# Kernel optimization log

Measured on AMD Instinct MI355X. Metric: run time of the kernel, lower is better.

## Reference

```python
import jax, jax.numpy as jnp
import numpy as np

B, N, D, E = 256, 192, 512, 1024
H = E // 2          # MLP hidden = 512
K = 58              # round(0.3 * 192), hardcoded in the torch forward
EPS_L2 = 1e-8
EPS_BN = 1e-5


def setup_inputs() -> dict:
    key = jax.random.key(0)
    ks = jax.random.split(key, 8)
    s = 0.02
    return {
        "all_patch_embeddings": jax.random.normal(ks[0], (B, N, D), dtype=jnp.float32),
        "attention_map": jax.random.uniform(ks[1], (B, N + 1, N + 1), dtype=jnp.float32),
        # fc: Linear(D, E)
        "W_fc": jax.random.normal(ks[2], (E, D), dtype=jnp.float32) * s,
        "b_fc": jnp.zeros((E,), dtype=jnp.float32),
        # mlp layer 0: Linear(D, H) + BatchNorm1d(H) + ReLU
        "W1": jax.random.normal(ks[3], (H, D), dtype=jnp.float32) * s,
        "b1": jnp.zeros((H,), dtype=jnp.float32),
        "gamma1": jnp.ones((H,), dtype=jnp.float32),
        "beta1": jnp.zeros((H,), dtype=jnp.float32),
        # mlp layer 1: Linear(H, E) (no BN/ReLU applied on last layer)
        "W2": jax.random.normal(ks[4], (E, H), dtype=jnp.float32) * s,
        "b2": jnp.zeros((E,), dtype=jnp.float32),
    }


def reference(all_patch_embeddings, attention_map, W_fc, b_fc, W1, b1, gamma1, beta1, W2, b2):
    # CLS-row attention over the 192 patch tokens: [B, N]
    cls_attn = attention_map[:, 0, 1:]
    # torch.sort(descending)[...,:K] == top-k indices (batched, replaces python loop)
    _, idx = jax.lax.top_k(cls_attn, K)                      # [B, K] int32
    # batched gather replacing the per-sample index_select loop
    sel = jnp.take_along_axis(all_patch_embeddings, idx[:, :, None], axis=1)  # [B, K, D]
    # l2norm over last dim
    norm = jnp.sqrt(jnp.sum(sel * sel, axis=-1, keepdims=True)) + EPS_L2
    base = sel / norm
    # .half() cast in the original (round-trip to fp16 precision)
    base = base.astype(jnp.float16).astype(jnp.float32)
    # fc branch
    feat_fc = jnp.einsum('bkd,ed->bke', base, W_fc) + b_fc    # [B, K, E]
    # mlp branch (num_layers=2): Linear -> BN(train-mode batch stats) -> ReLU -> Linear
    h = jnp.einsum('bkd,hd->bkh', base, W1) + b1              # [B, K, H]
    hf = h.reshape(B * K, H)
    mu = jnp.mean(hf, axis=0)
    var = jnp.var(hf, axis=0)
    hf = (hf - mu) * jax.lax.rsqrt(var + EPS_BN) * gamma1 + beta1
    h = jax.nn.relu(hf).reshape(B, K, H)
    feat_mlp = jnp.einsum('bkh,eh->bke', h, W2) + b2          # [B, K, E]
    feats = feat_mlp + feat_fc
    # maxk_pool1d_var with k=1 and lengths == K reduces to max over token dim
    return jnp.max(feats, axis=1).astype(jnp.float32)         # [B, E]
```

## Files before the change

kernel.cpp:

```cpp
#include <hip/hip_runtime.h>
#include <hip/hip_fp16.h>

#define B_ 256
#define N_ 192
#define D_ 512
#define E_ 1024
#define H_ 512
#define K_ 58
#define M_ (B_*K_)
#define M2_ (B_*64)

typedef _Float16 f16;
typedef unsigned int u32;
typedef _Float16 half8 __attribute__((ext_vector_type(8)));
typedef float floatx4 __attribute__((ext_vector_type(4)));

__device__ inline half8 cvt8(float4 f0, float4 f1) {
  half8 r;
  r[0]=(f16)f0.x; r[1]=(f16)f0.y; r[2]=(f16)f0.z; r[3]=(f16)f0.w;
  r[4]=(f16)f1.x; r[5]=(f16)f1.y; r[6]=(f16)f1.z; r[7]=(f16)f1.w;
  return r;
}

__device__ inline void gl_lds16(const f16* g, f16* l) {
  __builtin_amdgcn_global_load_lds((const __attribute__((address_space(1))) u32*)g,
                                   (__attribute__((address_space(3))) u32*)l, 16, 0, 0);
}

__device__ inline void stage128(const f16* gbase, int gstride, f16* sT, int w, int lane) {
  int lrow  = lane >> 2;
  int chunk = (lane & 3) ^ ((lane >> 3) & 3);
  gl_lds16(gbase + (size_t)(w*16      + lrow)*gstride + chunk*8, &sT[(w*16)*32]);
  gl_lds16(gbase + (size_t)(64 + w*16 + lrow)*gstride + chunk*8, &sT[(64 + w*16)*32]);
}

__global__ void setup_kernel(const float* __restrict__ Wfc, const float* __restrict__ W2,
                             const float* __restrict__ W1, const float* __restrict__ attn,
                             const float* __restrict__ emb,
                             f16* __restrict__ Wcat, f16* __restrict__ W1_16,
                             f16* __restrict__ A16, float* __restrict__ csum) {
  __shared__ float sv[N_];
  __shared__ int sidx[K_];
  __shared__ int cnt;
  int blk = blockIdx.x, t = threadIdx.x;
  if (blk < 512) {
    int idx = (blk*256 + t)*8;
    int e = idx >> 10, c = idx & 1023;
    const float* src = (c < 512) ? (Wfc + (size_t)e*512 + c)
                                 : (W2  + (size_t)e*512 + (c-512));
    half8 o = cvt8(((const float4*)src)[0], ((const float4*)src)[1]);
    *(uint4*)(Wcat + idx) = *(uint4*)&o;
  } else if (blk < 640) {
    int idx = ((blk-512)*256 + t)*8;
    const float* src = W1 + idx;
    half8 o = cvt8(((const float4*)src)[0], ((const float4*)src)[1]);
    *(uint4*)(W1_16 + idx) = *(uint4*)&o;
  } else if (blk < 896) {
    int b = blk - 640;
    if (t == 0) cnt = 0;
    if (t < N_) sv[t] = attn[(size_t)b*193*193 + 1 + t];
    __syncthreads();
    if (t < N_) {
      float v = sv[t]; int rank = 0;
      for (int j = 0; j < N_; ++j) {
        float vj = sv[j];
        rank += (vj > v) || (vj == v && j < t);
      }
      if (rank < K_) sidx[atomicAdd(&cnt, 1)] = t;
    }
    __syncthreads();
    int w = t >> 6, lane = t & 63;
    for (int slot = w; slot < 64; slot += 4) {
      f16* dst = A16 + ((size_t)b*64 + slot)*1024 + lane*8;
      if (slot < K_) {
        const float* src = emb + ((size_t)b*N_ + sidx[slot])*D_ + lane*8;
        float4 v0 = ((const float4*)src)[0];
        float4 v1 = ((const float4*)src)[1];
        float s = v0.x*v0.x + v0.y*v0.y + v0.z*v0.z + v0.w*v0.w
                + v1.x*v1.x + v1.y*v1.y + v1.z*v1.z + v1.w*v1.w;
        #pragma unroll
        for (int off = 32; off > 0; off >>= 1) s += __shfl_xor(s, off);
        float inv = 1.0f / (sqrtf(s) + 1e-8f);
        half8 o;
        o[0]=(f16)(v0.x*inv); o[1]=(f16)(v0.y*inv); o[2]=(f16)(v0.z*inv); o[3]=(f16)(v0.w*inv);
        o[4]=(f16)(v1.x*inv); o[5]=(f16)(v1.y*inv); o[6]=(f16)(v1.z*inv); o[7]=(f16)(v1.w*inv);
        *(uint4*)dst = *(uint4*)&o;
      } else {
        uint4 z; z.x=0u; z.y=0u; z.z=0u; z.w=0u;
        *(uint4*)dst = z;
      }
    }
  } else {
    float4 z; z.x=0.f; z.y=0.f; z.z=0.f; z.w=0.f;
    ((float4*)csum)[t] = z;
  }
}

__launch_bounds__(256)
__global__ void gemm1_kernel(const f16* __restrict__ A16, const f16* __restrict__ W1_16,
                             const float* __restrict__ b1, f16* __restrict__ Aout,
                             float* __restrict__ csum, float* __restrict__ css) {
  __shared__ f16 sA[2][128*32];
  __shared__ f16 sB[2][128*32];
  __shared__ float sSum[4][64], sSS[4][64];
  int t = threadIdx.x;
  int n0 = blockIdx.x * 128;
  int m0 = blockIdx.y * 128;
  int lane = t & 63, w = t >> 6, lm = lane & 15, quad = lane >> 4;
  int rh = w & 1, ch = w >> 1;
  floatx4 acc[4][4] = {};
  const f16* Ab = A16 + (size_t)m0*1024;
  const f16* Bb = W1_16 + (size_t)n0*512;
  int sw = (quad ^ ((lm >> 1) & 3)) * 8;
  stage128(Ab, 1024, sA[0], w, lane);
  stage128(Bb, 512,  sB[0], w, lane);
  __syncthreads();
  for (int it = 0; it < 16; ++it) {
    int cur = it & 1, nxt = cur ^ 1;
    if (it < 15) {
      stage128(Ab + (it+1)*32, 1024, sA[nxt], w, lane);
      stage128(Bb + (it+1)*32, 512,  sB[nxt], w, lane);
    }
    half8 a[4], bf[4];
    #pragma unroll
    for (int i = 0; i < 4; ++i) a[i]  = *(const half8*)&sA[cur][(rh*64 + i*16 + lm)*32 + sw];
    #pragma unroll
    for (int j = 0; j < 4; ++j) bf[j] = *(const half8*)&sB[cur][(ch*64 + j*16 + lm)*32 + sw];
    #pragma unroll
    for (int i = 0; i < 4; ++i)
      #pragma unroll
      for (int j = 0; j < 4; ++j)
        acc[i][j] = __builtin_amdgcn_mfma_f32_16x16x32_f16(a[i], bf[j], acc[i][j], 0, 0, 0);
    __syncthreads();
  }
  #pragma unroll
  for (int j = 0; j < 4; ++j) {
    int col = n0 + ch*64 + j*16 + lm;
    float bias = b1[col];
    float s = 0.f, ss = 0.f;
    #pragma unroll
    for (int i = 0; i < 4; ++i) {
      int rib = i*16 + quad*4;
      int row = m0 + rh*64 + rib;
      #pragma unroll
      for (int r = 0; r < 4; ++r) {
        float x = acc[i][j][r] + bias;
        Aout[(size_t)(row + r)*1024 + 512 + col] = (f16)x;
        if (rib + r < K_) { s += x; ss += x*x; }
      }
    }
    s  += __shfl_xor(s, 16);  s  += __shfl_xor(s, 32);
    ss += __shfl_xor(ss, 16); ss += __shfl_xor(ss, 32);
    if (lane < 16) { sSum[w][j*16 + lm] = s; sSS[w][j*16 + lm] = ss; }
  }
  __syncthreads();
  if (t < 128) {
    int wp = (t >> 6) * 2, ci = t & 63;
    atomicAdd(&csum[n0 + t], sSum[wp][ci] + sSum[wp+1][ci]);
    atomicAdd(&css[n0 + t],  sSS[wp][ci]  + sSS[wp+1][ci]);
  }
}

__global__ void bnrelu_kernel(f16* __restrict__ A16, const float* __restrict__ csum,
                              const float* __restrict__ css, const float* __restrict__ gamma,
                              const float* __restrict__ beta) {
  __shared__ float sSc[H_], sSh[H_];
  int t = threadIdx.x;
  for (int j = t; j < H_; j += 256) {
    float mu  = csum[j] * (1.0f/M_);
    float var = css[j] * (1.0f/M_) - mu*mu;
    float sc  = gamma[j] * rsqrtf(var + 1e-5f);
    sSc[j] = sc;
    sSh[j] = beta[j] - mu*sc;
  }
  __syncthreads();
  int r0 = blockIdx.x * 16;
  #pragma unroll
  for (int i = 0; i < 4; ++i) {
    int seg = t + 256*i;
    int row = r0 + (seg >> 6);
    int c0  = (seg & 63) * 8;
    f16* p = A16 + (size_t)row*1024 + 512 + c0;
    if ((row & 63) >= K_) {
      uint4 z; z.x=0u; z.y=0u; z.z=0u; z.w=0u;
      *(uint4*)p = z;
    } else {
      half8 hv = *(const half8*)p;
      half8 o;
      #pragma unroll
      for (int k = 0; k < 8; ++k)
        o[k] = (f16)fmaxf((float)hv[k]*sSc[c0+k] + sSh[c0+k], 0.0f);
      *(uint4*)p = *(uint4*)&o;
    }
  }
}

__launch_bounds__(256)
__global__ void fused_kernel(const f16* __restrict__ A16, const f16* __restrict__ Wcat,
                             const float* __restrict__ bfc, const float* __restrict__ b2,
                             float* __restrict__ out) {
  __shared__ f16 sA[2][128*32];
  __shared__ f16 sB[2][128*32];
  __shared__ float sMax[4][64];
  int t = threadIdx.x;
  int e0 = blockIdx.x * 128;
  int bm = blockIdx.y;
  int lane = t & 63, w = t >> 6, lm = lane & 15, quad = lane >> 4;
  int rh = w & 1, ch = w >> 1;
  floatx4 acc[4][4] = {};
  const f16* Ab = A16 + (size_t)bm*128*1024;
  const f16* Bb = Wcat + (size_t)e0*1024;
  int sw = (quad ^ ((lm >> 1) & 3)) * 8;
  stage128(Ab, 1024, sA[0], w, lane);
  stage128(Bb, 1024, sB[0], w, lane);
  __syncthreads();
  for (int it = 0; it < 32; ++it) {
    int cur = it & 1, nxt = cur ^ 1;
    if (it < 31) {
      stage128(Ab + (it+1)*32, 1024, sA[nxt], w, lane);
      stage128(Bb + (it+1)*32, 1024, sB[nxt], w, lane);
    }
    half8 a[4], bf[4];
    #pragma unroll
    for (int i = 0; i < 4; ++i) a[i]  = *(const half8*)&sA[cur][(rh*64 + i*16 + lm)*32 + sw];
    #pragma unroll
    for (int j = 0; j < 4; ++j) bf[j] = *(const half8*)&sB[cur][(ch*64 + j*16 + lm)*32 + sw];
    #pragma unroll
    for (int i = 0; i < 4; ++i)
      #pragma unroll
      for (int j = 0; j < 4; ++j)
        acc[i][j] = __builtin_amdgcn_mfma_f32_16x16x32_f16(a[i], bf[j], acc[i][j], 0, 0, 0);
    __syncthreads();
  }
  #pragma unroll
  for (int j = 0; j < 4; ++j) {
    float mx = -3.0e38f;
    #pragma unroll
    for (int i = 0; i < 4; ++i) {
      int rib = i*16 + quad*4;
      #pragma unroll
      for (int r = 0; r < 4; ++r)
        if (rib + r < K_) mx = fmaxf(mx, acc[i][j][r]);
    }
    mx = fmaxf(mx, __shfl_xor(mx, 16));
    mx = fmaxf(mx, __shfl_xor(mx, 32));
    if (lane < 16) sMax[w][j*16 + lm] = mx;
  }
  __syncthreads();
  {
    int bb = t >> 7, c = t & 127;
    float mx = sMax[(c >> 6)*2 + bb][c & 63];
    int e = e0 + c;
    out[((size_t)bm*2 + bb)*E_ + e] = mx + bfc[e] + b2[e];
  }
}

extern "C" void kernel_launch(void* const* d_in, const int* in_sizes, int n_in,
                              void* d_out, int out_size, void* d_ws, size_t ws_size,
                              hipStream_t stream) {
  const float* emb   = (const float*)d_in[0];
  const float* attn  = (const float*)d_in[1];
  const float* Wfc   = (const float*)d_in[2];
  const float* bfc   = (const float*)d_in[3];
  const float* W1    = (const float*)d_in[4];
  const float* b1    = (const float*)d_in[5];
  const float* gamma = (const float*)d_in[6];
  const float* beta  = (const float*)d_in[7];
  const float* W2    = (const float*)d_in[8];
  const float* b2    = (const float*)d_in[9];
  float* out = (float*)d_out;

  char* ws = (char*)d_ws;
  f16*   A16   = (f16*)(ws);
  f16*   Wcat  = (f16*)(ws + 33554432);
  f16*   W1_16 = (f16*)(ws + 35651584);
  float* csum  = (float*)(ws + 36175872);
  float* css   = (float*)(ws + 36177920);

  setup_kernel<<<897, 256, 0, stream>>>(Wfc, W2, W1, attn, emb, Wcat, W1_16, A16, csum);
  gemm1_kernel<<<dim3(H_/128, M2_/128), 256, 0, stream>>>(A16, W1_16, b1, A16, csum, css);
  bnrelu_kernel<<<M2_/16, 256, 0, stream>>>(A16, csum, css, gamma, beta);
  fused_kernel<<<dim3(E_/128, M2_/128), 256, 0, stream>>>(A16, Wcat, bfc, b2, out);
}
```

Measured before the change: 249.9 us.

## Widen GEMM tiles to 128x256 and remap blocks for XCD-aware locality

Both GEMM kernels now compute 128x256 output tiles per block, so each wave holds a 4x8 grid of MFMA accumulators. This halves A-tile reloads and raises the arithmetic intensity per LDS read. The launch switches to a 1D grid whose block-to-tile mapping places blocks sharing the same A rows on the same XCD (blockIdx & 7), aiming for better L2 reuse. In exchange, register pressure and LDS use go up, and block count halves (256 and 512 blocks), which may limit occupancy and wave-level parallelism.

New measurement: 248.6 us. No clear change (-0.5%).

```diff
diff --git a/kernel.cpp b/kernel.cpp
--- a/kernel.cpp
+++ b/kernel.cpp
@@ -32,6 +32,13 @@
   int chunk = (lane & 3) ^ ((lane >> 3) & 3);
   gl_lds16(gbase + (size_t)(w*16      + lrow)*gstride + chunk*8, &sT[(w*16)*32]);
   gl_lds16(gbase + (size_t)(64 + w*16 + lrow)*gstride + chunk*8, &sT[(64 + w*16)*32]);
+}
+__device__ inline void stage256(const f16* gbase, int gstride, f16* sT, int w, int lane) {
+  int lrow  = lane >> 2;
+  int chunk = (lane & 3) ^ ((lane >> 3) & 3);
+  #pragma unroll
+  for (int q = 0; q < 4; ++q)
+    gl_lds16(gbase + (size_t)(q*64 + w*16 + lrow)*gstride + chunk*8, &sT[(q*64 + w*16)*32]);
 }
 
 __global__ void setup_kernel(const float* __restrict__ Wfc, const float* __restrict__ W2,
@@ -96,52 +103,55 @@
   }
 }
 
-__launch_bounds__(256)
+__launch_bounds__(256, 2)
 __global__ void gemm1_kernel(const f16* __restrict__ A16, const f16* __restrict__ W1_16,
                              const float* __restrict__ b1, f16* __restrict__ Aout,
                              float* __restrict__ csum, float* __restrict__ css) {
   __shared__ f16 sA[2][128*32];
-  __shared__ f16 sB[2][128*32];
-  __shared__ float sSum[4][64], sSS[4][64];
+  __shared__ f16 sB[2][256*32];
+  __shared__ float sSum[4][128], sSS[4][128];
   int t = threadIdx.x;
-  int n0 = blockIdx.x * 128;
-  int m0 = blockIdx.y * 128;
+  int g = blockIdx.x;
+  int xcd = g & 7, rest = g >> 3;
+  int n0 = (rest & 1) * 256;
+  int m  = xcd + 8*(rest >> 1);
+  int m0 = m * 128;
   int lane = t & 63, w = t >> 6, lm = lane & 15, quad = lane >> 4;
-  int rh = w & 1, ch = w >> 1;
-  floatx4 acc[4][4] = {};
+  int rw = w & 1, cw = w >> 1;
+  floatx4 acc[4][8] = {};
   const f16* Ab = A16 + (size_t)m0*1024;
   const f16* Bb = W1_16 + (size_t)n0*512;
   int sw = (quad ^ ((lm >> 1) & 3)) * 8;
   stage128(Ab, 1024, sA[0], w, lane);
-  stage128(Bb, 512,  sB[0], w, lane);
+  stage256(Bb, 512,  sB[0], w, lane);
   __syncthreads();
   for (int it = 0; it < 16; ++it) {
     int cur = it & 1, nxt = cur ^ 1;
     if (it < 15) {
       stage128(Ab + (it+1)*32, 1024, sA[nxt], w, lane);
-      stage128(Bb + (it+1)*32, 512,  sB[nxt], w, lane);
-    }
-    half8 a[4], bf[4];
-    #pragma unroll
-    for (int i = 0; i < 4; ++i) a[i]  = *(const half8*)&sA[cur][(rh*64 + i*16 + lm)*32 + sw];
-    #pragma unroll
-    for (int j = 0; j < 4; ++j) bf[j] = *(const half8*)&sB[cur][(ch*64 + j*16 + lm)*32 + sw];
+      stage256(Bb + (it+1)*32, 512,  sB[nxt], w, lane);
+    }
+    half8 a[4], bf[8];
+    #pragma unroll
+    for (int i = 0; i < 4; ++i) a[i]  = *(const half8*)&sA[cur][(rw*64  + i*16 + lm)*32 + sw];
+    #pragma unroll
+    for (int j = 0; j < 8; ++j) bf[j] = *(const half8*)&sB[cur][(cw*128 + j*16 + lm)*32 + sw];
     #pragma unroll
     for (int i = 0; i < 4; ++i)
       #pragma unroll
-      for (int j = 0; j < 4; ++j)
+      for (int j = 0; j < 8; ++j)
         acc[i][j] = __builtin_amdgcn_mfma_f32_16x16x32_f16(a[i], bf[j], acc[i][j], 0, 0, 0);
     __syncthreads();
   }
   #pragma unroll
-  for (int j = 0; j < 4; ++j) {
-    int col = n0 + ch*64 + j*16 + lm;
+  for (int j = 0; j < 8; ++j) {
+    int col = n0 + cw*128 + j*16 + lm;
     float bias = b1[col];
     float s = 0.f, ss = 0.f;
     #pragma unroll
     for (int i = 0; i < 4; ++i) {
       int rib = i*16 + quad*4;
-      int row = m0 + rh*64 + rib;
+      int row = m0 + rw*64 + rib;
       #pragma unroll
       for (int r = 0; r < 4; ++r) {
         float x = acc[i][j][r] + bias;
@@ -154,10 +164,11 @@
     if (lane < 16) { sSum[w][j*16 + lm] = s; sSS[w][j*16 + lm] = ss; }
   }
   __syncthreads();
-  if (t < 128) {
-    int wp = (t >> 6) * 2, ci = t & 63;
-    atomicAdd(&csum[n0 + t], sSum[wp][ci] + sSum[wp+1][ci]);
-    atomicAdd(&css[n0 + t],  sSS[wp][ci]  + sSS[wp+1][ci]);
+  {
+    int c = t;
+    int w0 = 2*(c >> 7), ci = c & 127;
+    atomicAdd(&csum[n0 + c], sSum[w0][ci] + sSum[w0+1][ci]);
+    atomicAdd(&css[n0 + c],  sSS[w0][ci]  + sSS[w0+1][ci]);
   }
 }
 
@@ -195,45 +206,47 @@
   }
 }
 
-__launch_bounds__(256)
+__launch_bounds__(256, 2)
 __global__ void fused_kernel(const f16* __restrict__ A16, const f16* __restrict__ Wcat,
                              const float* __restrict__ bfc, const float* __restrict__ b2,
                              float* __restrict__ out) {
   __shared__ f16 sA[2][128*32];
-  __shared__ f16 sB[2][128*32];
-  __shared__ float sMax[4][64];
+  __shared__ f16 sB[2][256*32];
+  __shared__ float sMax[4][128];
   int t = threadIdx.x;
-  int e0 = blockIdx.x * 128;
-  int bm = blockIdx.y;
+  int g = blockIdx.x;
+  int xcd = g & 7, rest = g >> 3;
+  int e0 = (rest & 3) * 256;
+  int bm = xcd + 8*(rest >> 2);
   int lane = t & 63, w = t >> 6, lm = lane & 15, quad = lane >> 4;
-  int rh = w & 1, ch = w >> 1;
-  floatx4 acc[4][4] = {};
+  int rw = w & 1, cw = w >> 1;
+  floatx4 acc[4][8] = {};
   const f16* Ab = A16 + (size_t)bm*128*1024;
   const f16* Bb = Wcat + (size_t)e0*1024;
   int sw = (quad ^ ((lm >> 1) & 3)) * 8;
   stage128(Ab, 1024, sA[0], w, lane);
-  stage128(Bb, 1024, sB[0], w, lane);
+  stage256(Bb, 1024, sB[0], w, lane);
   __syncthreads();
   for (int it = 0; it < 32; ++it) {
     int cur = it & 1, nxt = cur ^ 1;
     if (it < 31) {
       stage128(Ab + (it+1)*32, 1024, sA[nxt], w, lane);
-      stage128(Bb + (it+1)*32, 1024, sB[nxt], w, lane);
-    }
-    half8 a[4], bf[4];
-    #pragma unroll
-    for (int i = 0; i < 4; ++i) a[i]  = *(const half8*)&sA[cur][(rh*64 + i*16 + lm)*32 + sw];
-    #pragma unroll
-    for (int j = 0; j < 4; ++j) bf[j] = *(const half8*)&sB[cur][(ch*64 + j*16 + lm)*32 + sw];
+      stage256(Bb + (it+1)*32, 1024, sB[nxt], w, lane);
+    }
+    half8 a[4], bf[8];
+    #pragma unroll
+    for (int i = 0; i < 4; ++i) a[i]  = *(const half8*)&sA[cur][(rw*64  + i*16 + lm)*32 + sw];
+    #pragma unroll
+    for (int j = 0; j < 8; ++j) bf[j] = *(const half8*)&sB[cur][(cw*128 + j*16 + lm)*32 + sw];
     #pragma unroll
     for (int i = 0; i < 4; ++i)
       #pragma unroll
-      for (int j = 0; j < 4; ++j)
+      for (int j = 0; j < 8; ++j)
         acc[i][j] = __builtin_amdgcn_mfma_f32_16x16x32_f16(a[i], bf[j], acc[i][j], 0, 0, 0);
     __syncthreads();
   }
   #pragma unroll
-  for (int j = 0; j < 4; ++j) {
+  for (int j = 0; j < 8; ++j) {
     float mx = -3.0e38f;
     #pragma unroll
     for (int i = 0; i < 4; ++i) {
@@ -247,9 +260,10 @@
     if (lane < 16) sMax[w][j*16 + lm] = mx;
   }
   __syncthreads();
-  {
-    int bb = t >> 7, c = t & 127;
-    float mx = sMax[(c >> 6)*2 + bb][c & 63];
+  #pragma unroll
+  for (int bb = 0; bb < 2; ++bb) {
+    int c = t;
+    float mx = sMax[bb + 2*(c >> 7)][c & 127];
     int e = e0 + c;
     out[((size_t)bm*2 + bb)*E_ + e] = mx + bfc[e] + b2[e];
   }
@@ -278,7 +292,7 @@
   float* css   = (float*)(ws + 36177920);
 
   setup_kernel<<<897, 256, 0, stream>>>(Wfc, W2, W1, attn, emb, Wcat, W1_16, A16, csum);
-  gemm1_kernel<<<dim3(H_/128, M2_/128), 256, 0, stream>>>(A16, W1_16, b1, A16, csum, css);
+  gemm1_kernel<<<256, 256, 0, stream>>>(A16, W1_16, b1, A16, csum, css);
   bnrelu_kernel<<<M2_/16, 256, 0, stream>>>(A16, csum, css, gamma, beta);
-  fused_kernel<<<dim3(E_/128, M2_/128), 256, 0, stream>>>(A16, Wcat, bfc, b2, out);
-}
+  fused_kernel<<<512, 256, 0, stream>>>(A16, Wcat, bfc, b2, out);
+}
```
